# Kernel optimization log

Measured on AMD Instinct MI355X. Metric: run time of the kernel, lower is better.

Reference implementation:

```python
import jax, jax.numpy as jnp
import numpy as np

H = 16  # n_heads

def _split_heads(x, n_heads):
    B, S, Dm = x.shape
    return x.reshape(B, S, n_heads, Dm // n_heads).transpose(0, 2, 1, 3)  # [B,H,S,D]

def _matmul_prefix_sum(x, y, z):
    """Faithful, efficient form of the TF matmul_prefix_sum.
    TF builds yz[s] = y[s] (x) z[s] outer products, cumsums over s, then
    contracts with x[t]/ (t+1).  That equals a causal-masked bilinear form:
      out[t, j] = (1/(t+1)) * sum_{s<=t} (x[t]. y[s]) * z[s, j]
    so we compute (x y^T * tril / idx) @ z without the 5D intermediate.
    """
    S = x.shape[2]
    idx = jnp.arange(1, S + 1, dtype=x.dtype)[:, None]        # position 1..S
    mask = jnp.tril(jnp.ones((S, S), dtype=x.dtype))
    scores = jnp.einsum('bhtd,bhsd->bhts', x, y) * (mask / idx)
    return jnp.einsum('bhts,bhsj->bhtj', scores, z)

def setup_inputs() -> dict:
    key = jax.random.key(0)
    ks = jax.random.split(key, 12)
    B, S, Dm = 2, 1024, 1024
    f32 = jnp.float32
    rn = lambda k, shp: jax.random.normal(k, shp, dtype=f32)
    w_scale = f32(1.0 / np.sqrt(Dm))
    return {
        'v': rn(ks[0], (B, S, Dm)),
        'k': rn(ks[1], (B, S, Dm)),
        'q': rn(ks[2], (B, S, Dm)),
        'p': rn(ks[3], (B, S, Dm)),
        'wq_k': rn(ks[4], (Dm, Dm)) * w_scale, 'wq_b': jnp.zeros((Dm,), f32),
        'wk_k': rn(ks[5], (Dm, Dm)) * w_scale, 'wk_b': jnp.zeros((Dm,), f32),
        'wv_k': rn(ks[6], (Dm, Dm)) * w_scale, 'wv_b': jnp.zeros((Dm,), f32),
        'wc_k': rn(ks[7], (Dm, Dm)) * w_scale, 'wc_b': jnp.zeros((Dm,), f32),
    }

def reference(v, k, q, p, wq_k, wq_b, wk_k, wk_b, wv_k, wv_b, wc_k, wc_b):
    B, S, Dm = q.shape
    D = Dm // H
    norm_d = 1.0 / jnp.sqrt(jnp.asarray(D, q.dtype))
    ph = _split_heads(p, H)                                    # [B,H,S,D]
    qh = _split_heads((q @ wq_k + wq_b) * norm_d, H)
    kh = _split_heads(k @ wk_k + wk_b, H)
    vh = _split_heads(v @ wv_k + wv_b, H)
    # elu(p q^T)+1 then transpose -> indexed [B,H,t(query),s(p-position)]
    attn_pack = jax.nn.elu(jnp.einsum('bhtd,bhsd->bhts', qh, ph)) + 1.0
    attn_unpack = _matmul_prefix_sum(qh, kh, attn_pack)        # [B,H,S,S]
    attn_unpack = jax.nn.softmax(attn_unpack, axis=-1)
    attn_out = _matmul_prefix_sum(attn_unpack, attn_pack, vh)  # [B,H,S,D]
    attn_out = attn_out.transpose(0, 2, 1, 3).reshape(B, S, Dm)
    return attn_out @ wc_k + wc_b
```

## Files before the change

### kernel.cpp

```cpp
#include <hip/hip_runtime.h>

#define DEVI static __device__ __forceinline__

using s16x8 = __attribute__((ext_vector_type(8))) short;
using f32x4 = __attribute__((ext_vector_type(4))) float;
using u32x4 = __attribute__((ext_vector_type(4))) unsigned int;

static constexpr int H  = 16;
static constexpr int S  = 1024;
static constexpr int DM = 1024;
static constexpr int NB = 2;
static constexpr int BS = NB * S;
static constexpr long SS  = (long)S * S;
static constexpr long HSS = (long)H * SS;
static constexpr long SDM = (long)S * DM;

DEVI unsigned short f2bf(float f) {
    union { float f; unsigned u; } c; c.f = f;
    c.u += 0x7FFFu + ((c.u >> 16) & 1u);
    return (unsigned short)(c.u >> 16);
}
DEVI float bf2f(unsigned short v) {
    union { unsigned u; float f; } c; c.u = ((unsigned)v) << 16;
    return c.f;
}

DEVI void gload16(const unsigned short* g, unsigned short* l) {
    __builtin_amdgcn_global_load_lds(
        (const __attribute__((address_space(1))) unsigned int*)g,
        (__attribute__((address_space(3))) unsigned int*)l, 16, 0, 0);
}

enum { EPI_BFB = 0, EPI_VTB, EPI_PACK, EPI_PACK2, EPI_MASK, EPI_BF, EPI_OUT };

__global__ __launch_bounds__(256)
void gemmU(const unsigned short* __restrict__ Aall,
           const unsigned short* __restrict__ Ball,
           unsigned short* __restrict__ Oall)
{
    const int L = (int)blockIdx.x + ((int)blockIdx.y << 3) + ((int)blockIdx.z << 6);
    const int g = L & 7, r = L >> 3;
    const int bz = g + ((r >> 6) << 3);
    const int bx = r & 7;
    const int by = 7 - ((r >> 3) & 7);
    const int m0 = by * 128, n0 = bx * 128;
    const unsigned short* Ap = Aall + (long)bz * SS;
    const unsigned short* Bp = Ball + (long)bz * SS;

    __shared__ alignas(16) unsigned short lA[128 * 64];
    __shared__ alignas(16) unsigned short lB[128 * 64];

    const int tid = threadIdx.x, w = tid >> 6, lane = tid & 63;
    const int lr = lane & 15, lg = lane >> 4;
    const int wm = (w >> 1) << 6, wn = (w & 1) << 6;

    const unsigned short* gA[4]; const unsigned short* gB[4]; int lo[4];
#pragma unroll
    for (int i = 0; i < 4; ++i) {
        const int q = (i * 4 + w) * 64 + lane, row = q >> 3, slot = q & 7;
        const int gs = (slot ^ (row & 7)) * 8;
        gA[i] = Ap + (long)(m0 + row) * S + gs;
        gB[i] = Bp + (long)(n0 + row) * S + gs;
        lo[i] = (i * 4 + w) * 512;
    }

    int abase[4], axor[4], bbase[4], bxor[4];
#pragma unroll
    for (int f = 0; f < 4; ++f) {
        const int ra = wm + f * 16 + lr;
        abase[f] = ra * 64; axor[f] = (ra & 7) * 8;
        const int rb = wn + f * 16 + lr;
        bbase[f] = rb * 64; bxor[f] = (rb & 7) * 8;
    }

    f32x4 acc[4][4] = {};
    const int Keff = m0 + 128;

    for (int k0 = 0; k0 < Keff; k0 += 64) {
#pragma unroll
        for (int i = 0; i < 4; ++i) {
            gload16(gA[i] + k0, &lA[lo[i]]);
            gload16(gB[i] + k0, &lB[lo[i]]);
        }
        __syncthreads();
#pragma unroll
        for (int kk = 0; kk < 64; kk += 32) {
            s16x8 af[4], bv[4];
#pragma unroll
            for (int f = 0; f < 4; ++f) {
                af[f] = *reinterpret_cast<const s16x8*>(&lA[abase[f] + ((kk + 8 * lg) ^ axor[f])]);
                bv[f] = *reinterpret_cast<const s16x8*>(&lB[bbase[f] + ((kk + 8 * lg) ^ bxor[f])]);
            }
#pragma unroll
            for (int fm = 0; fm < 4; ++fm)
#pragma unroll
                for (int fn = 0; fn < 4; ++fn)
                    acc[fm][fn] = __builtin_amdgcn_mfma_f32_16x16x32_bf16(af[fm], bv[fn], acc[fm][fn], 0, 0, 0);
        }
        __syncthreads();
    }

    const long obase = (long)bz * SS;
#pragma unroll
    for (int fm = 0; fm < 4; ++fm)
#pragma unroll
        for (int fn = 0; fn < 4; ++fn) {
            const int t0 = m0 + wm + fm * 16 + lg * 4;
            const int gn = n0 + wn + fn * 16 + lr;
#pragma unroll
            for (int rr = 0; rr < 4; ++rr)
                Oall[obase + (long)(t0 + rr) * S + gn] = f2bf(__expf(acc[fm][fn][rr]));
        }
}

__global__ __launch_bounds__(256)
void gemmV(const unsigned short* __restrict__ Aall,
           const unsigned short* __restrict__ Ball,
           unsigned short* __restrict__ Oall, const float* __restrict__ inv2)
{
    const int L = (int)blockIdx.x + ((int)blockIdx.y << 3) + ((int)blockIdx.z << 6);
    const int g = L & 7, r = L >> 3;
    const int bz = g + ((r >> 6) << 3);
    const int bx = r & 7;
    const int by = 7 - ((r >> 3) & 7);
    const int m0 = by * 128, n0 = bx * 128;
    if (n0 > m0 + 127) return;
    const unsigned short* Ap = Aall + (long)bz * SS;
    const unsigned short* Bp = Ball + (long)bz * SS;

    __shared__ alignas(16) unsigned short lA[128 * 64];
    __shared__ alignas(16) unsigned short lB[128 * 64];

    const int tid = threadIdx.x, w = tid >> 6, lane = tid & 63;
    const int lr = lane & 15, lg = lane >> 4;
    const int wm = (w >> 1) << 6, wn = (w & 1) << 6;

    const unsigned short* gA[4]; const unsigned short* gB[4]; int lo[4];
#pragma unroll
    for (int i = 0; i < 4; ++i) {
        const int q = (i * 4 + w) * 64 + lane, row = q >> 3, slot = q & 7;
        const int gs = (slot ^ (row & 7)) * 8;
        gA[i] = Ap + (long)(m0 + row) * S + gs;
        gB[i] = Bp + (long)(n0 + row) * S + gs;
        lo[i] = (i * 4 + w) * 512;
    }

    int abase[4], axor[4], bbase[4], bxor[4];
#pragma unroll
    for (int f = 0; f < 4; ++f) {
        const int ra = wm + f * 16 + lr;
        abase[f] = ra * 64; axor[f] = (ra & 7) * 8;
        const int rb = wn + f * 16 + lr;
        bbase[f] = rb * 64; bxor[f] = (rb & 7) * 8;
    }

    f32x4 acc[4][4] = {};

    for (int k0 = 0; k0 < S; k0 += 64) {
#pragma unroll
        for (int i = 0; i < 4; ++i) {
            gload16(gA[i] + k0, &lA[lo[i]]);
            gload16(gB[i] + k0, &lB[lo[i]]);
        }
        __syncthreads();
#pragma unroll
        for (int kk = 0; kk < 64; kk += 32) {
            s16x8 af[4], bv[4];
#pragma unroll
            for (int f = 0; f < 4; ++f) {
                af[f] = *reinterpret_cast<const s16x8*>(&lA[abase[f] + ((kk + 8 * lg) ^ axor[f])]);
                bv[f] = *reinterpret_cast<const s16x8*>(&lB[bbase[f] + ((kk + 8 * lg) ^ bxor[f])]);
            }
#pragma unroll
            for (int fm = 0; fm < 4; ++fm)
#pragma unroll
                for (int fn = 0; fn < 4; ++fn)
                    acc[fm][fn] = __builtin_amdgcn_mfma_f32_16x16x32_bf16(af[fm], bv[fn], acc[fm][fn], 0, 0, 0);
        }
        __syncthreads();
    }

    const long obase = (long)bz * SS;
#pragma unroll
    for (int fm = 0; fm < 4; ++fm) {
        const int t0 = m0 + wm + fm * 16 + lg * 4;
        float rec[4];
#pragma unroll
        for (int rr = 0; rr < 4; ++rr)
            rec[rr] = inv2[(long)bz * S + t0 + rr];
#pragma unroll
        for (int fn = 0; fn < 4; ++fn) {
            const int gn = n0 + wn + fn * 16 + lr;
#pragma unroll
            for (int rr = 0; rr < 4; ++rr) {
                const int gm = t0 + rr;
                const float vv = (gn <= gm) ? acc[fm][fn][rr] * rec[rr] : 0.f;
                Oall[obase + (long)gm * S + gn] = f2bf(vv);
            }
        }
    }
}

template<int TM, int TN, int EPI, bool CK, bool CS, bool SWZ, bool REVY>
__global__ __launch_bounds__((TM/64)*(TN/64)*64)
void gemmT(const unsigned short* __restrict__ Aall, long a_sb, long a_sh, int lda,
           const unsigned short* __restrict__ Ball, long b_sb, long b_sh, int ldb,
           void* __restrict__ Oall, void* __restrict__ O2, long o_sb, long o_sh, int ldo,
           const float* __restrict__ bias, int bstride, int K, int NV)
{
    constexpr int WN = TN / 64, WM = TM / 64, NWV = WM * WN, NTHR = NWV * 64;
    constexpr int IA = (TM * 8) / NTHR, IB = (TN * 8) / NTHR;

    int bx, by, bz;
    if (SWZ) {
        const int L = (int)blockIdx.x + ((int)blockIdx.y << 3) + ((int)blockIdx.z << 6);
        const int g = L & 7, r = L >> 3;
        bz = g + ((r >> 6) << 3);
        bx = r & 7;
        by = 7 - ((r >> 3) & 7);
    } else {
        bx = blockIdx.x;
        by = REVY ? (int)gridDim.y - 1 - (int)blockIdx.y : (int)blockIdx.y;
        bz = blockIdx.z;
    }
    const int m0 = by * TM, n0 = bx * TN;
    if (CS && n0 > m0 + TM - 1) return;
    const int zb = bz >> 4, zh = bz & 15;
    const unsigned short* Ap = Aall + (long)zb * a_sb + (long)zh * a_sh;
    const unsigned short* Bp = Ball + (long)zb * b_sb + (long)zh * b_sh;
    const float* bi = bias + (long)zh * bstride;

    __shared__ alignas(16) unsigned short lA[TM * 64];
    __shared__ alignas(16) unsigned short lB[TN * 64];

    const int tid = threadIdx.x, w = tid >> 6, lane = tid & 63;
    const int lr = lane & 15, lg = lane >> 4;
    const int wm = (w / WN) * 64, wn = (w % WN) * 64;

    const unsigned short* gA[IA]; int loA[IA];
    const unsigned short* gB[IB]; int loB[IB];
#pragma unroll
    for (int i = 0; i < IA; ++i) {
        const int q = i * NTHR + tid, row = q >> 3, slot = q & 7;
        gA[i]  = Ap + (long)(m0 + row) * lda + ((slot ^ (row & 7)) * 8);
        loA[i] = (i * NWV + w) * 512;
    }
#pragma unroll
    for (int i = 0; i < IB; ++i) {
        const int q = i * NTHR + tid, row = q >> 3, slot = q & 7;
        int rb = n0 + row; if (rb >= NV) rb = NV - 1;
        gB[i]  = Bp + (long)rb * ldb + ((slot ^ (row & 7)) * 8);
        loB[i] = (i * NWV + w) * 512;
    }

    int abase[4], axor[4], bbase[4], bxor[4];
#pragma unroll
    for (int f = 0; f < 4; ++f) {
        const int ra = wm + f * 16 + lr;
        abase[f] = ra * 64; axor[f] = (ra & 7) * 8;
        const int rb = wn + f * 16 + lr;
        bbase[f] = rb * 64; bxor[f] = (rb & 7) * 8;
    }

    f32x4 acc[4][4] = {};
    const int Keff = CK ? ((K < m0 + TM) ? K : m0 + TM) : K;

    for (int k0 = 0; k0 < Keff; k0 += 64) {
#pragma unroll
        for (int i = 0; i < IA; ++i) gload16(gA[i] + k0, &lA[loA[i]]);
#pragma unroll
        for (int i = 0; i < IB; ++i) gload16(gB[i] + k0, &lB[loB[i]]);
        __syncthreads();
#pragma unroll
        for (int kk = 0; kk < 64; kk += 32) {
            s16x8 af[4], bv[4];
#pragma unroll
            for (int f = 0; f < 4; ++f) {
                af[f] = *reinterpret_cast<const s16x8*>(&lA[abase[f] + ((kk + 8 * lg) ^ axor[f])]);
                bv[f] = *reinterpret_cast<const s16x8*>(&lB[bbase[f] + ((kk + 8 * lg) ^ bxor[f])]);
            }
#pragma unroll
            for (int fm = 0; fm < 4; ++fm)
#pragma unroll
                for (int fn = 0; fn < 4; ++fn)
                    acc[fm][fn] = __builtin_amdgcn_mfma_f32_16x16x32_bf16(af[fm], bv[fn], acc[fm][fn], 0, 0, 0);
        }
        __syncthreads();
    }

    const long obase = (long)zb * o_sb + (long)zh * o_sh;
#pragma unroll
    for (int fm = 0; fm < 4; ++fm)
#pragma unroll
        for (int fn = 0; fn < 4; ++fn) {
            const int t0 = m0 + wm + fm * 16 + lg * 4;
            const int gn = n0 + wn + fn * 16 + lr;
            if (gn >= NV) continue;
            if constexpr (EPI == EPI_PACK2) {
                ushort4 pt;
                unsigned short* o1 = (unsigned short*)Oall;
                unsigned short* o2 = (unsigned short*)O2;
#pragma unroll
                for (int r = 0; r < 4; ++r) {
                    float vv = acc[fm][fn][r];
                    vv = vv > 0.f ? vv + 1.f : __expf(vv);
                    const unsigned short b = f2bf(vv);
                    o1[obase + (long)(t0 + r) * ldo + gn] = b;
                    ((unsigned short*)&pt)[r] = b;
                }
                *reinterpret_cast<ushort4*>(&o2[obase + (long)gn * ldo + t0]) = pt;
            } else {
#pragma unroll
                for (int r = 0; r < 4; ++r) {
                    const int gm = t0 + r;
                    float vv = acc[fm][fn][r];
                    const long o = obase + (long)gm * ldo + gn;
                    if constexpr (EPI == EPI_BFB) {
                        ((unsigned short*)Oall)[o] = f2bf(vv + bi[gn]);
                    } else if constexpr (EPI == EPI_VTB) {
                        ((unsigned short*)Oall)[o] = f2bf(vv + bi[gm]);
                    } else if constexpr (EPI == EPI_PACK) {
                        vv = vv > 0.f ? vv + 1.f : __expf(vv);
                        ((unsigned short*)Oall)[o] = f2bf(vv);
                    } else if constexpr (EPI == EPI_MASK) {
                        vv = (gn <= gm) ? vv / (float)(gm + 1) : 0.f;
                        ((unsigned short*)Oall)[o] = f2bf(vv);
                    } else if constexpr (EPI == EPI_BF) {
                        ((unsigned short*)Oall)[o] = f2bf(vv);
                    } else {
                        ((float*)Oall)[o] = vv + bi[gn];
                    }
                }
            }
        }
}

__global__ __launch_bounds__(256)
void packsqk(const unsigned short* __restrict__ qh,
             const unsigned short* __restrict__ pbf,
             const unsigned short* __restrict__ kh,
             unsigned short* __restrict__ P, unsigned short* __restrict__ PT,
             unsigned short* __restrict__ SQ)
{
    const int L = (int)blockIdx.x + ((int)blockIdx.y << 3) + ((int)blockIdx.z << 6);
    const int g = L & 7, r = L >> 3;
    const int bzz = g + ((r >> 6) << 3);
    const int bx = r & 7, by = 7 - ((r >> 3) & 7);
    const int job = bzz >> 5, zz = bzz & 31;
    const int m0 = by * 128, n0 = bx * 128;
    if (job && n0 > m0 + 127) return;
    const int zb = zz >> 4, zh = zz & 15;
    const unsigned short* Ap = qh + (long)zb * SDM + zh * 64;
    const unsigned short* Bp = (job ? kh : pbf) + (long)zb * SDM + zh * 64;

    __shared__ alignas(16) unsigned short lA[128 * 64];
    __shared__ alignas(16) unsigned short lB[128 * 64];

    const int tid = threadIdx.x, w = tid >> 6, lane = tid & 63;
    const int lr = lane & 15, lg = lane >> 4;
    const int wm = (w >> 1) << 6, wn = (w & 1) << 6;

#pragma unroll
    for (int i = 0; i < 4; ++i) {
        const int q = i * 256 + tid, row = q >> 3, slot = q & 7;
        const int gs = (slot ^ (row & 7)) * 8;
        gload16(Ap + (long)(m0 + row) * DM + gs, &lA[(i * 4 + w) * 512]);
        gload16(Bp + (long)(n0 + row) * DM + gs, &lB[(i * 4 + w) * 512]);
    }
    __syncthreads();

    f32x4 acc[4][4] = {};
#pragma unroll
    for (int kk = 0; kk < 64; kk += 32) {
        s16x8 af[4], bv[4];
#pragma unroll
        for (int f = 0; f < 4; ++f) {
            const int ra = wm + f * 16 + lr;
            af[f] = *reinterpret_cast<const s16x8*>(&lA[ra * 64 + ((kk + 8 * lg) ^ ((ra & 7) * 8))]);
            const int rb = wn + f * 16 + lr;
            bv[f] = *reinterpret_cast<const s16x8*>(&lB[rb * 64 + ((kk + 8 * lg) ^ ((rb & 7) * 8))]);
        }
#pragma unroll
        for (int fm = 0; fm < 4; ++fm)
#pragma unroll
            for (int fn = 0; fn < 4; ++fn)
                acc[fm][fn] = __builtin_amdgcn_mfma_f32_16x16x32_bf16(af[fm], bv[fn], acc[fm][fn], 0, 0, 0);
    }

    const long obase = (long)zz * SS;
#pragma unroll
    for (int fm = 0; fm < 4; ++fm)
#pragma unroll
        for (int fn = 0; fn < 4; ++fn) {
            const int t0 = m0 + wm + fm * 16 + lg * 4;
            const int gn = n0 + wn + fn * 16 + lr;
            if (job == 0) {
                ushort4 pt;
#pragma unroll
                for (int rr = 0; rr < 4; ++rr) {
                    float vv = acc[fm][fn][rr];
                    vv = vv > 0.f ? vv + 1.f : __expf(vv);
                    const unsigned short b = f2bf(vv);
                    P[obase + (long)(t0 + rr) * S + gn] = b;
                    ((unsigned short*)&pt)[rr] = b;
                }
                *reinterpret_cast<ushort4*>(&PT[obase + (long)gn * S + t0]) = pt;
            } else {
#pragma unroll
                for (int rr = 0; rr < 4; ++rr) {
                    const int gm = t0 + rr;
                    float vv = acc[fm][fn][rr];
                    vv = (gn <= gm) ? vv / (float)(gm + 1) : 0.f;
                    SQ[obase + (long)gm * S + gn] = f2bf(vv);
                }
            }
        }
}

__global__ __launch_bounds__(256)
void rowsum_inv(const unsigned short* __restrict__ E, float* __restrict__ inv2)
{
    const int w = threadIdx.x >> 6, lane = threadIdx.x & 63;
    const long row = (long)blockIdx.x * 4 + w;
    const u32x4* r4 = reinterpret_cast<const u32x4*>(E + row * S);
    u32x4 a = r4[lane * 2], b = r4[lane * 2 + 1];
    float s = 0.f;
#pragma unroll
    for (int i = 0; i < 4; ++i) {
        s += bf2f((unsigned short)(a[i] & 0xFFFF)) + bf2f((unsigned short)(a[i] >> 16));
        s += bf2f((unsigned short)(b[i] & 0xFFFF)) + bf2f((unsigned short)(b[i] >> 16));
    }
#pragma unroll
    for (int off = 32; off; off >>= 1) s += __shfl_xor(s, off);
    if (lane == 0) inv2[row] = 1.f / (s * (float)((row & (S - 1)) + 1));
}

__global__ __launch_bounds__(256)
void prep(const float* __restrict__ q_in, const float* __restrict__ k_in,
          const float* __restrict__ v_in, const float* __restrict__ p_in,
          const float* __restrict__ wq, const float* __restrict__ wk,
          const float* __restrict__ wv, const float* __restrict__ wc,
          const float* __restrict__ wqb, const float* __restrict__ wkb,
          unsigned short* __restrict__ qbf, unsigned short* __restrict__ wqT,
          float* __restrict__ bq2, int n4)
{
    const int z = blockIdx.z, bx = blockIdx.x, tid = threadIdx.x;
    if (z < 4) {
        const int i = bx * 256 + tid;
        if (i >= n4) return;
        const float* s = (z == 0) ? q_in : (z == 1) ? k_in : (z == 2) ? v_in : p_in;
        float4 x = reinterpret_cast<const float4*>(s)[i];
        ushort4 o; o.x = f2bf(x.x); o.y = f2bf(x.y); o.z = f2bf(x.z); o.w = f2bf(x.w);
        reinterpret_cast<ushort4*>(qbf + (size_t)z * n4 * 4)[i] = o;
    } else if (z < 8) {
        if (bx >= 256) return;
        __shared__ unsigned short t[64][72];
        const int zz = z - 4;
        const float* src = (zz == 0) ? wq : (zz == 1) ? wk : (zz == 2) ? wv : wc;
        const float scale = (zz == 0) ? 0.125f : 1.0f;
        unsigned short* dst = wqT + (size_t)zz * DM * DM;
        const int r0 = (bx >> 4) * 64, c0 = (bx & 15) * 64;
        const int lrow = tid >> 2, lseg = (tid & 3) << 4;
        const float4* g4 = reinterpret_cast<const float4*>(src + (long)(r0 + lrow) * DM + c0 + lseg);
        alignas(16) unsigned short tmp[16];
#pragma unroll
        for (int qq = 0; qq < 4; ++qq) {
            float4 x = g4[qq];
            tmp[4*qq+0] = f2bf(x.x * scale); tmp[4*qq+1] = f2bf(x.y * scale);
            tmp[4*qq+2] = f2bf(x.z * scale); tmp[4*qq+3] = f2bf(x.w * scale);
        }
#pragma unroll
        for (int j = 0; j < 16; ++j) t[lrow][lseg + j] = tmp[j];
        __syncthreads();
#pragma unroll
        for (int j = 0; j < 16; ++j) tmp[j] = t[lseg + j][lrow];
        unsigned short* d = dst + (long)(c0 + lrow) * DM + r0 + lseg;
        *reinterpret_cast<u32x4*>(d)     = *reinterpret_cast<const u32x4*>(tmp);
        *reinterpret_cast<u32x4*>(d + 8) = *reinterpret_cast<const u32x4*>(tmp + 8);
    } else {
        if (bx >= 4) return;
        const int i = bx * 256 + tid;
        if (i < DM) { bq2[i] = wqb[i] * 0.125f; bq2[DM + i] = wkb[i]; }
    }
}

extern "C" void kernel_launch(void* const* d_in, const int* in_sizes, int n_in,
                              void* d_out, int out_size, void* d_ws, size_t ws_size,
                              hipStream_t stream)
{
    (void)in_sizes; (void)n_in; (void)out_size;
    const float* v_in = (const float*)d_in[0];
    const float* k_in = (const float*)d_in[1];
    const float* q_in = (const float*)d_in[2];
    const float* p_in = (const float*)d_in[3];
    const float* wq   = (const float*)d_in[4];
    const float* wqb  = (const float*)d_in[5];
    const float* wk   = (const float*)d_in[6];
    const float* wkb  = (const float*)d_in[7];
    const float* wvw  = (const float*)d_in[8];
    const float* wvb  = (const float*)d_in[9];
    const float* wc   = (const float*)d_in[10];
    const float* wcb  = (const float*)d_in[11];
    float* out = (float*)d_out;

    char* ws = (char*)d_ws;
    size_t off = 0;
    auto take = [&](size_t n) { char* p = ws + off; off += (n + 255) & ~(size_t)255; return p; };
    unsigned short* qbf = (unsigned short*)take((size_t)BS * DM * 2);
    unsigned short* kbf = (unsigned short*)take((size_t)BS * DM * 2);
    unsigned short* vbf = (unsigned short*)take((size_t)BS * DM * 2);
    unsigned short* pbf = (unsigned short*)take((size_t)BS * DM * 2);
    unsigned short* wqT = (unsigned short*)take((size_t)DM * DM * 2);
    unsigned short* wkT = (unsigned short*)take((size_t)DM * DM * 2);
    unsigned short* wvT = (unsigned short*)take((size_t)DM * DM * 2);
    unsigned short* wcT = (unsigned short*)take((size_t)DM * DM * 2);
    float*          bq2 = (float*)take((size_t)2 * DM * 4);
    float*          inv = (float*)take((size_t)NB * H * S * 4);
    unsigned short* qh  = (unsigned short*)take((size_t)BS * DM * 2);
    unsigned short* kh  = (unsigned short*)take((size_t)BS * DM * 2);
    unsigned short* vhT = (unsigned short*)take((size_t)BS * DM * 2);
    unsigned short* ao  = (unsigned short*)take((size_t)BS * DM * 2);
    const size_t ssz = (size_t)NB * HSS * 2;
    unsigned short* B1 = (unsigned short*)take(ssz);
    unsigned short* B2 = (unsigned short*)take(ssz);
    unsigned short* B3 = (unsigned short*)take(ssz);
    const bool dual = (ws_size >= off + ssz);
    unsigned short* B4 = dual ? (unsigned short*)take(ssz) : nullptr;
    (void)kbf; (void)wkT;

    const int n4 = BS * DM / 4;
    const dim3 b256(256), b128(128), b64(64);

    prep<<<dim3(n4 / 256, 1, 9), b256, 0, stream>>>(
        q_in, k_in, v_in, p_in, wq, wk, wvw, wc, wqb, wkb, qbf, wqT, bq2, n4);

    gemmT<64,128,EPI_BFB,false,false,false,false><<<dim3(8, 32, 2), b128, 0, stream>>>(
        qbf, 0, (long)BS*DM, DM,  wqT, 0, (long)DM*DM, DM,  qh, nullptr, 0, (long)BS*DM, DM,
        bq2, DM, DM, DM);
    gemmT<64,128,EPI_VTB,false,false,false,false><<<dim3(8, 16, 2), b128, 0, stream>>>(
        wvT, 0, 0, DM,  vbf, 0, SDM, DM,  vhT, nullptr, 0, (long)DM*S, S,
        wvb, 0, DM, S);

    unsigned short *pbuf, *ptbuf, *sqkbuf, *ebuf, *s2buf;
    if (dual) {
        packsqk<<<dim3(8, 8, 64), b256, 0, stream>>>(qh, pbf, kh, B1, B2, B3);
        pbuf = B1; ptbuf = B2; sqkbuf = B3; ebuf = B4; s2buf = B3;
    } else {
        gemmT<128,128,EPI_PACK,false,false,true,false><<<dim3(8, 8, 32), b256, 0, stream>>>(
            pbf, SDM, 64, DM,  qh, SDM, 64, DM,  B1, nullptr, HSS, SS, S,  wvb, 0, 64, S);
        gemmT<128,128,EPI_MASK,false,true,true,false><<<dim3(8, 8, 32), b256, 0, stream>>>(
            qh, SDM, 64, DM,  kh, SDM, 64, DM,  B2, nullptr, HSS, SS, S,  wvb, 0, 64, S);
        ptbuf = B1; sqkbuf = B2; ebuf = B3; pbuf = B1; s2buf = B2;
    }
    gemmU<<<dim3(8, 8, 32), b256, 0, stream>>>(sqkbuf, ptbuf, ebuf);
    rowsum_inv<<<dim3(NB*H*S/4), b256, 0, stream>>>(ebuf, inv);
    if (!dual) {
        gemmT<128,128,EPI_PACK,false,false,true,false><<<dim3(8, 8, 32), b256, 0, stream>>>(
            qh, SDM, 64, DM,  pbf, SDM, 64, DM,  B1, nullptr, HSS, SS, S,  wvb, 0, 64, S);
    }
    gemmV<<<dim3(8, 8, 32), b256, 0, stream>>>(ebuf, pbuf, s2buf, inv);
    gemmT<64,64,EPI_BF,true,false,false,true><<<dim3(1, 16, 32), b64, 0, stream>>>(
        s2buf, HSS, SS, S,  vhT, (long)DM*S, (long)64*S, S,  ao, nullptr, SDM, 64, DM,
        wvb, 0, S, 64);
    gemmT<64,128,EPI_OUT,false,false,false,false><<<dim3(8, 32, 1), b128, 0, stream>>>(
        ao, 0, 0, DM,  wcT, 0, 0, DM,  out, nullptr, 0, 0, DM,  wcb, 0, DM, DM);
}
```

Baseline: 295.0 us.

## Fuse row-sum into exp GEMM epilogue and merge Q/V projections into one launch

The exp GEMM epilogue now reduces each row's exponentials across lanes and writes per-column-tile partial sums to a small buffer. A tiny finalize kernel adds the 16 partials and computes the inverse normaliser. This replaces the separate rowsum pass that re-read the whole 64 MB bf16 exp matrix. In addition, the Q projection and the transposed V projection GEMMs are merged into one kernel launch dispatched on blockIdx.z. The partial sums now come from unrounded fp32 values, not bf16-rounded ones, so the normaliser differs slightly from the value implied by the stored matrix.

```diff
diff --git a/kernel.cpp b/kernel.cpp
--- a/kernel.cpp
+++ b/kernel.cpp
@@ -36,7 +36,7 @@
 __global__ __launch_bounds__(256)
 void gemmU(const unsigned short* __restrict__ Aall,
            const unsigned short* __restrict__ Ball,
-           unsigned short* __restrict__ Oall)
+           unsigned short* __restrict__ Oall, float* __restrict__ psum)
 {
     const int L = (int)blockIdx.x + ((int)blockIdx.y << 3) + ((int)blockIdx.z << 6);
     const int g = L & 7, r = L >> 3;
@@ -101,16 +101,29 @@
     }
 
     const long obase = (long)bz * SS;
-#pragma unroll
-    for (int fm = 0; fm < 4; ++fm)
+    float* ps = psum + ((long)bz * 16 + bx * 2 + (w & 1)) * S;
+#pragma unroll
+    for (int fm = 0; fm < 4; ++fm) {
+        const int t0 = m0 + wm + fm * 16 + lg * 4;
+        float es[4] = {0.f, 0.f, 0.f, 0.f};
 #pragma unroll
         for (int fn = 0; fn < 4; ++fn) {
-            const int t0 = m0 + wm + fm * 16 + lg * 4;
             const int gn = n0 + wn + fn * 16 + lr;
 #pragma unroll
-            for (int rr = 0; rr < 4; ++rr)
-                Oall[obase + (long)(t0 + rr) * S + gn] = f2bf(__expf(acc[fm][fn][rr]));
-        }
+            for (int rr = 0; rr < 4; ++rr) {
+                const float e = __expf(acc[fm][fn][rr]);
+                Oall[obase + (long)(t0 + rr) * S + gn] = f2bf(e);
+                es[rr] += e;
+            }
+        }
+#pragma unroll
+        for (int rr = 0; rr < 4; ++rr) {
+            float s = es[rr];
+            s += __shfl_xor(s, 1); s += __shfl_xor(s, 2);
+            s += __shfl_xor(s, 4); s += __shfl_xor(s, 8);
+            if (lr == 0) ps[t0 + rr] = s;
+        }
+    }
 }
 
 __global__ __launch_bounds__(256)
@@ -199,6 +212,112 @@
             }
         }
     }
+}
+
+__global__ __launch_bounds__(256)
+void sumfin(const float* __restrict__ psum, float* __restrict__ inv2)
+{
+    const long i = (long)blockIdx.x * 256 + threadIdx.x;
+    const long bz = i >> 10, row = i & 1023;
+    const float* p = psum + (bz * 16) * S + row;
+    float s = 0.f;
+#pragma unroll
+    for (int k = 0; k < 16; ++k) s += p[(long)k * S];
+    inv2[bz * S + row] = 1.f / (s * (float)(row + 1));
+}
+
+__global__ __launch_bounds__(128)
+void proj3(const unsigned short* __restrict__ qbf,
+           const unsigned short* __restrict__ wqT,
+           const unsigned short* __restrict__ vbf,
+           const unsigned short* __restrict__ wvT,
+           const float* __restrict__ bq2, const float* __restrict__ wvb,
+           unsigned short* __restrict__ qh, unsigned short* __restrict__ vhT)
+{
+    const int z = blockIdx.z, bx = blockIdx.x, by = blockIdx.y;
+    const unsigned short *Ap, *Bp; unsigned short* Op;
+    const float* bi; int m0; bool vt;
+    if (z < 2) {
+        Ap = qbf + (long)z * BS * DM;  Bp = wqT + (long)z * DM * DM;
+        Op = qh  + (long)z * BS * DM;  bi = bq2 + z * DM;
+        m0 = by * 64; vt = false;
+    } else {
+        const int zb = by >> 4;
+        Ap = wvT;                      Bp = vbf + (long)zb * SDM;
+        Op = vhT + (long)zb * (long)DM * S;  bi = wvb;
+        m0 = (by & 15) * 64; vt = true;
+    }
+    const int n0 = bx * 128;
+
+    __shared__ alignas(16) unsigned short lA[64 * 64];
+    __shared__ alignas(16) unsigned short lB[128 * 64];
+
+    const int tid = threadIdx.x, w = tid >> 6, lane = tid & 63;
+    const int lr = lane & 15, lg = lane >> 4;
+    const int wn = (w & 1) << 6;
+
+    const unsigned short* gA[4]; int loA[4];
+    const unsigned short* gB[8]; int loB[8];
+#pragma unroll
+    for (int i = 0; i < 4; ++i) {
+        const int q = i * 128 + tid, row = q >> 3, slot = q & 7;
+        gA[i]  = Ap + (long)(m0 + row) * DM + ((slot ^ (row & 7)) * 8);
+        loA[i] = (i * 2 + w) * 512;
+    }
+#pragma unroll
+    for (int i = 0; i < 8; ++i) {
+        const int q = i * 128 + tid, row = q >> 3, slot = q & 7;
+        gB[i]  = Bp + (long)(n0 + row) * DM + ((slot ^ (row & 7)) * 8);
+        loB[i] = (i * 2 + w) * 512;
+    }
+
+    int abase[4], axor[4], bbase[4], bxor[4];
+#pragma unroll
+    for (int f = 0; f < 4; ++f) {
+        const int ra = f * 16 + lr;
+        abase[f] = ra * 64; axor[f] = (ra & 7) * 8;
+        const int rb = wn + f * 16 + lr;
+        bbase[f] = rb * 64; bxor[f] = (rb & 7) * 8;
+    }
+
+    f32x4 acc[4][4] = {};
+
+    for (int k0 = 0; k0 < DM; k0 += 64) {
+#pragma unroll
+        for (int i = 0; i < 4; ++i) gload16(gA[i] + k0, &lA[loA[i]]);
+#pragma unroll
+        for (int i = 0; i < 8; ++i) gload16(gB[i] + k0, &lB[loB[i]]);
+        __syncthreads();
+#pragma unroll
+        for (int kk = 0; kk < 64; kk += 32) {
+            s16x8 af[4], bv[4];
+#pragma unroll
+            for (int f = 0; f < 4; ++f) {
+                af[f] = *reinterpret_cast<const s16x8*>(&lA[abase[f] + ((kk + 8 * lg) ^ axor[f])]);
+                bv[f] = *reinterpret_cast<const s16x8*>(&lB[bbase[f] + ((kk + 8 * lg) ^ bxor[f])]);
+            }
+#pragma unroll
+            for (int fm = 0; fm < 4; ++fm)
+#pragma unroll
+                for (int fn = 0; fn < 4; ++fn)
+                    acc[fm][fn] = __builtin_amdgcn_mfma_f32_16x16x32_bf16(af[fm], bv[fn], acc[fm][fn], 0, 0, 0);
+        }
+        __syncthreads();
+    }
+
+#pragma unroll
+    for (int fm = 0; fm < 4; ++fm)
+#pragma unroll
+        for (int fn = 0; fn < 4; ++fn) {
+            const int t0 = m0 + fm * 16 + lg * 4;
+            const int gn = n0 + wn + fn * 16 + lr;
+#pragma unroll
+            for (int rr = 0; rr < 4; ++rr) {
+                const int gm = t0 + rr;
+                const float vv = acc[fm][fn][rr] + (vt ? bi[gm] : bi[gn]);
+                Op[(long)gm * 1024 + gn] = f2bf(vv);
+            }
+        }
 }
 
 template<int TM, int TN, int EPI, bool CK, bool CS, bool SWZ, bool REVY>
@@ -418,24 +537,6 @@
 }
 
 __global__ __launch_bounds__(256)
-void rowsum_inv(const unsigned short* __restrict__ E, float* __restrict__ inv2)
-{
-    const int w = threadIdx.x >> 6, lane = threadIdx.x & 63;
-    const long row = (long)blockIdx.x * 4 + w;
-    const u32x4* r4 = reinterpret_cast<const u32x4*>(E + row * S);
-    u32x4 a = r4[lane * 2], b = r4[lane * 2 + 1];
-    float s = 0.f;
-#pragma unroll
-    for (int i = 0; i < 4; ++i) {
-        s += bf2f((unsigned short)(a[i] & 0xFFFF)) + bf2f((unsigned short)(a[i] >> 16));
-        s += bf2f((unsigned short)(b[i] & 0xFFFF)) + bf2f((unsigned short)(b[i] >> 16));
-    }
-#pragma unroll
-    for (int off = 32; off; off >>= 1) s += __shfl_xor(s, off);
-    if (lane == 0) inv2[row] = 1.f / (s * (float)((row & (S - 1)) + 1));
-}
-
-__global__ __launch_bounds__(256)
 void prep(const float* __restrict__ q_in, const float* __restrict__ k_in,
           const float* __restrict__ v_in, const float* __restrict__ p_in,
           const float* __restrict__ wq, const float* __restrict__ wk,
@@ -516,6 +617,7 @@
     unsigned short* wcT = (unsigned short*)take((size_t)DM * DM * 2);
     float*          bq2 = (float*)take((size_t)2 * DM * 4);
     float*          inv = (float*)take((size_t)NB * H * S * 4);
+    float*          psum= (float*)take((size_t)NB * H * 16 * S * 4);
     unsigned short* qh  = (unsigned short*)take((size_t)BS * DM * 2);
     unsigned short* kh  = (unsigned short*)take((size_t)BS * DM * 2);
     unsigned short* vhT = (unsigned short*)take((size_t)BS * DM * 2);
@@ -534,12 +636,8 @@
     prep<<<dim3(n4 / 256, 1, 9), b256, 0, stream>>>(
         q_in, k_in, v_in, p_in, wq, wk, wvw, wc, wqb, wkb, qbf, wqT, bq2, n4);
 
-    gemmT<64,128,EPI_BFB,false,false,false,false><<<dim3(8, 32, 2), b128, 0, stream>>>(
-        qbf, 0, (long)BS*DM, DM,  wqT, 0, (long)DM*DM, DM,  qh, nullptr, 0, (long)BS*DM, DM,
-        bq2, DM, DM, DM);
-    gemmT<64,128,EPI_VTB,false,false,false,false><<<dim3(8, 16, 2), b128, 0, stream>>>(
-        wvT, 0, 0, DM,  vbf, 0, SDM, DM,  vhT, nullptr, 0, (long)DM*S, S,
-        wvb, 0, DM, S);
+    proj3<<<dim3(8, 32, 3), b128, 0, stream>>>(
+        qbf, wqT, vbf, wvT, bq2, wvb, qh, vhT);
 
     unsigned short *pbuf, *ptbuf, *sqkbuf, *ebuf, *s2buf;
     if (dual) {
@@ -552,8 +650,8 @@
             qh, SDM, 64, DM,  kh, SDM, 64, DM,  B2, nullptr, HSS, SS, S,  wvb, 0, 64, S);
         ptbuf = B1; sqkbuf = B2; ebuf = B3; pbuf = B1; s2buf = B2;
     }
-    gemmU<<<dim3(8, 8, 32), b256, 0, stream>>>(sqkbuf, ptbuf, ebuf);
-    rowsum_inv<<<dim3(NB*H*S/4), b256, 0, stream>>>(ebuf, inv);
+    gemmU<<<dim3(8, 8, 32), b256, 0, stream>>>(sqkbuf, ptbuf, ebuf, psum);
+    sumfin<<<dim3(NB*H*S/256), b256, 0, stream>>>(psum, inv);
     if (!dual) {
         gemmT<128,128,EPI_PACK,false,false,true,false><<<dim3(8, 8, 32), b256, 0, stream>>>(
             qh, SDM, 64, DM,  pbf, SDM, 64, DM,  B1, nullptr, HSS, SS, S,  wvb, 0, 64, S);
```

Result: faster. 275.4 us (median of 2 runs) (-6.6%).
